# Kernel optimization log

Hardware: AMD Instinct MI355X
Metric: run time of the kernel (lower is better)

Reference implementation:

```python
import jax, jax.numpy as jnp
import numpy as np

N = 100000
E = 300000
IN_C = 256
HID = 256   # 2 * out_channels
OUT_C = 128


def setup_inputs() -> dict:
    key = jax.random.key(0)
    k1, k2, k3, k4, k5 = jax.random.split(key, 5)
    x = jax.random.normal(k1, (N, IN_C), dtype=jnp.float32)
    edge_index = jax.random.randint(k2, (2, E), 0, N, dtype=jnp.int64)
    # Glorot-style init scale for GEMM weights
    W1 = jax.random.normal(k3, (IN_C, HID), dtype=jnp.float32) * (1.0 / np.sqrt(IN_C))
    b1 = jnp.zeros((HID,), dtype=jnp.float32)
    W2 = jax.random.normal(k4, (HID, OUT_C), dtype=jnp.float32) * (1.0 / np.sqrt(HID))
    b2 = jnp.zeros((OUT_C,), dtype=jnp.float32)
    return {"x": x, "edge_index": edge_index, "W1": W1, "b1": b1, "W2": W2, "b2": b2}


def _gcn_conv(x, W, b, src, dst, norm, n_nodes):
    # x: [N, Fin] -> transform then gather-scale-scatter aggregate
    h = x @ W                                   # [N, Fout]
    msgs = h[src] * norm[:, None]               # [E+N, Fout] (includes self-loops)
    out = jax.ops.segment_sum(msgs, dst, num_segments=n_nodes)
    return out + b


def _gcn_norm(edge_index, n_nodes):
    # add self-loops, compute symmetric deg^-1/2 normalization (PyG GCNConv default)
    loops = jnp.arange(n_nodes, dtype=edge_index.dtype)
    src = jnp.concatenate([edge_index[0], loops])
    dst = jnp.concatenate([edge_index[1], loops])
    deg = jax.ops.segment_sum(jnp.ones_like(dst, dtype=jnp.float32), dst, num_segments=n_nodes)
    dinv = jnp.where(deg > 0, jax.lax.rsqrt(deg), 0.0)
    norm = dinv[src] * dinv[dst]                # [E+N]
    return src, dst, norm


def reference(x, edge_index, W1, b1, W2, b2):
    n_nodes = x.shape[0]
    src, dst, norm = _gcn_norm(edge_index, n_nodes)
    h = _gcn_conv(x, W1, b1, src, dst, norm, n_nodes)
    h = jax.nn.relu(h)
    # dropout is identity in eval mode (reference baseline runs deterministic eval)
    return _gcn_conv(h, W2, b2, src, dst, norm, n_nodes)
```

## Files before the change

kernel.cpp:

```cpp
#include <hip/hip_runtime.h>
#include <stdint.h>

#define IN_C  256
#define HID   256
#define OUT_C 128
#define SCAN_BS 1024

typedef __bf16 bf16x8 __attribute__((ext_vector_type(8)));
typedef float  f32x4  __attribute__((ext_vector_type(4)));
typedef unsigned short u16x8 __attribute__((ext_vector_type(8)));
typedef unsigned short u16x4 __attribute__((ext_vector_type(4)));
typedef unsigned short u16x2 __attribute__((ext_vector_type(2)));
typedef unsigned int u32;

static __device__ __forceinline__ unsigned short f2b(float f) {
    union { float f; uint32_t u; } v; v.f = f;
    uint32_t r = v.u + 0x7fffu + ((v.u >> 16) & 1u);
    return (unsigned short)(r >> 16);
}
static __device__ __forceinline__ float b2f(unsigned short b) {
    union { uint32_t u; float f; } v; v.u = ((uint32_t)b) << 16;
    return v.f;
}

typedef __attribute__((address_space(1))) const u32 gas_u32;
typedef __attribute__((address_space(3))) u32 las_u32;
static __device__ __forceinline__ void gld16(const void* g, void* l) {
    __builtin_amdgcn_global_load_lds((gas_u32*)g, (las_u32*)l, 16, 0, 0);
}

__global__ void k_zero_i(int* __restrict__ p, int n) {
    int i = blockIdx.x * blockDim.x + threadIdx.x;
    if (i < n) p[i] = 0;
}

__global__ void k_count(const int* __restrict__ dst, int* __restrict__ cnt, int e) {
    int i = blockIdx.x * blockDim.x + threadIdx.x;
    if (i < e) atomicAdd(&cnt[dst[i]], 1);
}

__global__ __launch_bounds__(SCAN_BS) void k_scan_block(
    const int* __restrict__ cnt, int* __restrict__ rs, int* __restrict__ bsum, int n) {
    __shared__ int s[SCAN_BS];
    const int tid = threadIdx.x;
    const int i = blockIdx.x * SCAN_BS + tid;
    int v = (i < n) ? cnt[i] + 1 : 0;
    s[tid] = v;
    __syncthreads();
    for (int off = 1; off < SCAN_BS; off <<= 1) {
        int t = (tid >= off) ? s[tid - off] : 0;
        __syncthreads();
        s[tid] += t;
        __syncthreads();
    }
    if (i < n) rs[i] = s[tid] - v;
    if (tid == SCAN_BS - 1) bsum[blockIdx.x] = s[tid];
}

__global__ void k_scan_sums(int* __restrict__ bsum, int nb) {
    __shared__ int s[128];
    const int tid = threadIdx.x;
    int v = (tid < nb) ? bsum[tid] : 0;
    s[tid] = v;
    __syncthreads();
    for (int off = 1; off < 128; off <<= 1) {
        int t = (tid >= off) ? s[tid - off] : 0;
        __syncthreads();
        s[tid] += t;
        __syncthreads();
    }
    if (tid < nb) bsum[tid] = s[tid] - v;
}

__global__ void k_scan_add(int* __restrict__ rs, int* __restrict__ cur,
                           const int* __restrict__ bsum, const int* __restrict__ cnt,
                           float* __restrict__ dinv, int2* __restrict__ csrw, int n) {
    int i = blockIdx.x * blockDim.x + threadIdx.x;
    if (i < n) {
        int v = rs[i] + bsum[i >> 10];
        rs[i] = v;
        cur[i] = v + 1;
        float dp1 = (float)(cnt[i] + 1);
        dinv[i] = rsqrtf(dp1);
        csrw[v] = make_int2(i, __float_as_int(1.0f / dp1));
    }
}

__global__ void k_fill(const int* __restrict__ src, const int* __restrict__ dst,
                       const float* __restrict__ dinv,
                       int* __restrict__ cur, int2* __restrict__ csrw, int e) {
    int i = blockIdx.x * blockDim.x + threadIdx.x;
    if (i < e) {
        int s = src[i], d = dst[i];
        int p = atomicAdd(&cur[d], 1);
        csrw[p] = make_int2(s, __float_as_int(dinv[s] * dinv[d]));
    }
}

__global__ void k_prep(const float* __restrict__ W1, const float* __restrict__ W2,
                       unsigned short* __restrict__ W1T, unsigned short* __restrict__ W2T) {
    int i = blockIdx.x * blockDim.x + threadIdx.x;
    if (i < 65536) W1T[i] = f2b(W1[(i & 255) * HID + (i >> 8)]);
    if (i < 32768) W2T[i] = f2b(W2[(i & 255) * OUT_C + (i >> 8)]);
}

__global__ __launch_bounds__(512) void k_gemm1(
    const float* __restrict__ x, const unsigned short* __restrict__ W1T,
    unsigned short* __restrict__ t1, int n) {
    __shared__ __align__(16) unsigned short As[128 * 64];
    __shared__ __align__(16) unsigned short Bs[256 * 64];
    const int tid  = threadIdx.x;
    const int row0 = blockIdx.x * 128;
    const int wid = tid >> 6, lane = tid & 63;
    const int wm = wid >> 2, wn = wid & 3;
    const int lrow = lane & 15, lgrp = lane >> 4;

    f32x4 acc[4][4];
    #pragma unroll
    for (int i = 0; i < 4; ++i)
        #pragma unroll
        for (int j = 0; j < 4; ++j)
            acc[i][j] = (f32x4){0.f, 0.f, 0.f, 0.f};

    for (int kt = 0; kt < 4; ++kt) {
        #pragma unroll
        for (int i = 0; i < 4; ++i) {
            int chunk = tid + 512 * i;
            int nn = chunk >> 3, c = chunk & 7;
            gld16(&W1T[(size_t)nn * 256 + kt * 64 + ((c ^ (nn & 7)) * 8)],
                  &Bs[chunk * 8]);
        }
        #pragma unroll
        for (int i = 0; i < 2; ++i) {
            int chunk = tid + 512 * i;
            int r = chunk >> 3, c = chunk & 7;
            int grow = row0 + r;
            u16x8 pk = {0, 0, 0, 0, 0, 0, 0, 0};
            if (grow < n) {
                const float* sp = x + (size_t)grow * IN_C + kt * 64 + c * 8;
                float4 a = *(const float4*)sp;
                float4 b = *(const float4*)(sp + 4);
                pk[0] = f2b(a.x); pk[1] = f2b(a.y); pk[2] = f2b(a.z); pk[3] = f2b(a.w);
                pk[4] = f2b(b.x); pk[5] = f2b(b.y); pk[6] = f2b(b.z); pk[7] = f2b(b.w);
            }
            *(u16x8*)&As[r * 64 + ((c ^ (r & 7)) * 8)] = pk;
        }
        __syncthreads();
        #pragma unroll
        for (int kk = 0; kk < 2; ++kk) {
            const int cfrag = kk * 4 + lgrp;
            bf16x8 av[4], bv[4];
            #pragma unroll
            for (int mf = 0; mf < 4; ++mf) {
                int r = wm * 64 + mf * 16 + lrow;
                av[mf] = *(const bf16x8*)&As[r * 64 + ((cfrag ^ (r & 7)) * 8)];
            }
            #pragma unroll
            for (int nf = 0; nf < 4; ++nf) {
                int cc = wn * 64 + nf * 16 + lrow;
                bv[nf] = *(const bf16x8*)&Bs[cc * 64 + ((cfrag ^ (cc & 7)) * 8)];
            }
            #pragma unroll
            for (int mf = 0; mf < 4; ++mf)
                #pragma unroll
                for (int nf = 0; nf < 4; ++nf)
                    acc[mf][nf] = __builtin_amdgcn_mfma_f32_16x16x32_bf16(
                        av[mf], bv[nf], acc[mf][nf], 0, 0, 0);
        }
        __syncthreads();
    }
    #pragma unroll
    for (int mf = 0; mf < 4; ++mf)
        #pragma unroll
        for (int j = 0; j < 4; ++j) {
            int grow = row0 + wm * 64 + mf * 16 + lgrp * 4 + j;
            if (grow < n) {
                #pragma unroll
                for (int nf = 0; nf < 4; ++nf) {
                    int col = wn * 64 + nf * 16 + lrow;
                    t1[(size_t)grow * HID + col] = f2b(acc[mf][nf][j]);
                }
            }
        }
}

__global__ __launch_bounds__(256) void k_agg1(
    const unsigned short* __restrict__ t1, const int* __restrict__ rs,
    const int* __restrict__ cnt, const int2* __restrict__ csrw,
    const float* __restrict__ b1, unsigned short* __restrict__ out1, int n) {
    const int w = blockIdx.x * 4 + (threadIdx.x >> 6);
    const int n0 = w * 4;
    if (n0 >= n) return;
    const int lane = threadIdx.x & 63;
    const int ch = lane * 4;
    int beg[4], m[4];
    #pragma unroll
    for (int q = 0; q < 4; ++q) {
        int node = n0 + q;
        bool valid = node < n;
        beg[q] = valid ? rs[node] : 0;
        m[q]   = valid ? cnt[node] + 1 : 0;
    }
    float acc[4][4];
    #pragma unroll
    for (int q = 0; q < 4; ++q)
        #pragma unroll
        for (int k = 0; k < 4; ++k) acc[q][k] = 0.f;
    const int m01 = m[0] > m[1] ? m[0] : m[1];
    const int m23 = m[2] > m[3] ? m[2] : m[3];
    const int mmax = m01 > m23 ? m01 : m23;
    for (int j = 0; j < mmax; ++j) {
        #pragma unroll
        for (int q = 0; q < 4; ++q) {
            if (j < m[q]) {
                int2 p = csrw[beg[q] + j];
                float wq = __int_as_float(p.y);
                u16x4 u = *(const u16x4*)&t1[(size_t)p.x * HID + ch];
                acc[q][0] += b2f(u[0]) * wq; acc[q][1] += b2f(u[1]) * wq;
                acc[q][2] += b2f(u[2]) * wq; acc[q][3] += b2f(u[3]) * wq;
            }
        }
    }
    float4 bb = *(const float4*)(b1 + ch);
    #pragma unroll
    for (int q = 0; q < 4; ++q) {
        int node = n0 + q;
        if (node < n) {
            u16x4 o;
            o[0] = f2b(fmaxf(acc[q][0] + bb.x, 0.f));
            o[1] = f2b(fmaxf(acc[q][1] + bb.y, 0.f));
            o[2] = f2b(fmaxf(acc[q][2] + bb.z, 0.f));
            o[3] = f2b(fmaxf(acc[q][3] + bb.w, 0.f));
            *(u16x4*)&out1[(size_t)node * HID + ch] = o;
        }
    }
}

__global__ __launch_bounds__(256) void k_gemm2(
    const unsigned short* __restrict__ out1, const unsigned short* __restrict__ W2T,
    unsigned short* __restrict__ t2, int n) {
    __shared__ __align__(16) unsigned short As[128 * 64];
    __shared__ __align__(16) unsigned short Bs[128 * 64];
    const int tid  = threadIdx.x;
    const int row0 = blockIdx.x * 128;
    const int wid = tid >> 6, lane = tid & 63;
    const int wm = wid >> 1, wn = wid & 1;
    const int lrow = lane & 15, lgrp = lane >> 4;

    f32x4 acc[4][4];
    #pragma unroll
    for (int i = 0; i < 4; ++i)
        #pragma unroll
        for (int j = 0; j < 4; ++j)
            acc[i][j] = (f32x4){0.f, 0.f, 0.f, 0.f};

    for (int kt = 0; kt < 4; ++kt) {
        #pragma unroll
        for (int i = 0; i < 4; ++i) {
            int chunk = tid + 256 * i;
            int r = chunk >> 3, c = chunk & 7;
            int grow = row0 + r; if (grow > n - 1) grow = n - 1;
            gld16(&out1[(size_t)grow * HID + kt * 64 + ((c ^ (r & 7)) * 8)],
                  &As[chunk * 8]);
        }
        #pragma unroll
        for (int i = 0; i < 4; ++i) {
            int chunk = tid + 256 * i;
            int nn = chunk >> 3, c = chunk & 7;
            gld16(&W2T[(size_t)nn * 256 + kt * 64 + ((c ^ (nn & 7)) * 8)],
                  &Bs[chunk * 8]);
        }
        __syncthreads();
        #pragma unroll
        for (int kk = 0; kk < 2; ++kk) {
            const int cfrag = kk * 4 + lgrp;
            bf16x8 av[4], bv[4];
            #pragma unroll
            for (int mf = 0; mf < 4; ++mf) {
                int r = wm * 64 + mf * 16 + lrow;
                av[mf] = *(const bf16x8*)&As[r * 64 + ((cfrag ^ (r & 7)) * 8)];
            }
            #pragma unroll
            for (int nf = 0; nf < 4; ++nf) {
                int cc = wn * 64 + nf * 16 + lrow;
                bv[nf] = *(const bf16x8*)&Bs[cc * 64 + ((cfrag ^ (cc & 7)) * 8)];
            }
            #pragma unroll
            for (int mf = 0; mf < 4; ++mf)
                #pragma unroll
                for (int nf = 0; nf < 4; ++nf)
                    acc[mf][nf] = __builtin_amdgcn_mfma_f32_16x16x32_bf16(
                        av[mf], bv[nf], acc[mf][nf], 0, 0, 0);
        }
        __syncthreads();
    }
    #pragma unroll
    for (int mf = 0; mf < 4; ++mf)
        #pragma unroll
        for (int j = 0; j < 4; ++j) {
            int grow = row0 + wm * 64 + mf * 16 + lgrp * 4 + j;
            if (grow < n) {
                #pragma unroll
                for (int nf = 0; nf < 4; ++nf) {
                    int col = wn * 64 + nf * 16 + lrow;
                    t2[(size_t)grow * OUT_C + col] = f2b(acc[mf][nf][j]);
                }
            }
        }
}

__global__ __launch_bounds__(256) void k_agg2(
    const unsigned short* __restrict__ t2, const int* __restrict__ rs,
    const int* __restrict__ cnt, const int2* __restrict__ csrw,
    const float* __restrict__ b2, float* __restrict__ out, int n) {
    const int w = blockIdx.x * 4 + (threadIdx.x >> 6);
    const int n0 = w * 4;
    if (n0 >= n) return;
    const int lane = threadIdx.x & 63;
    const int ch = lane * 2;
    int beg[4], m[4];
    #pragma unroll
    for (int q = 0; q < 4; ++q) {
        int node = n0 + q;
        bool valid = node < n;
        beg[q] = valid ? rs[node] : 0;
        m[q]   = valid ? cnt[node] + 1 : 0;
    }
    float acc[4][2];
    #pragma unroll
    for (int q = 0; q < 4; ++q) { acc[q][0] = 0.f; acc[q][1] = 0.f; }
    const int m01 = m[0] > m[1] ? m[0] : m[1];
    const int m23 = m[2] > m[3] ? m[2] : m[3];
    const int mmax = m01 > m23 ? m01 : m23;
    for (int j = 0; j < mmax; ++j) {
        #pragma unroll
        for (int q = 0; q < 4; ++q) {
            if (j < m[q]) {
                int2 p = csrw[beg[q] + j];
                float wq = __int_as_float(p.y);
                u16x2 u = *(const u16x2*)&t2[(size_t)p.x * OUT_C + ch];
                acc[q][0] += b2f(u[0]) * wq; acc[q][1] += b2f(u[1]) * wq;
            }
        }
    }
    float2 bb = *(const float2*)(b2 + ch);
    #pragma unroll
    for (int q = 0; q < 4; ++q) {
        int node = n0 + q;
        if (node < n)
            *(float2*)&out[(size_t)node * OUT_C + ch] =
                make_float2(acc[q][0] + bb.x, acc[q][1] + bb.y);
    }
}

extern "C" void kernel_launch(void* const* d_in, const int* in_sizes, int n_in,
                              void* d_out, int out_size, void* d_ws, size_t ws_size,
                              hipStream_t stream) {
    const float* x  = (const float*)d_in[0];
    const int*   ei = (const int*)d_in[1];
    const float* W1 = (const float*)d_in[2];
    const float* b1 = (const float*)d_in[3];
    const float* W2 = (const float*)d_in[4];
    const float* b2 = (const float*)d_in[5];
    float* out = (float*)d_out;

    const int n = in_sizes[0] / IN_C;
    const int e = in_sizes[1] / 2;
    const int* src = ei;
    const int* dst = ei + e;

    int*   cnt  = (int*)d_ws;
    int*   rs   = cnt + n;
    int*   cur  = rs + n;
    int*   bsum = cur + n;
    float* dinv = (float*)(bsum + 128);
    int2*  csrw = (int2*)(dinv + n);
    unsigned short* W1T = (unsigned short*)(csrw + (size_t)e + n);
    unsigned short* W2T = W1T + 65536;
    unsigned short* t1  = W2T + 32768;
    unsigned short* out1 = t1 + (size_t)n * HID;
    unsigned short* t2  = t1;

    const int nb = (n + SCAN_BS - 1) / SCAN_BS;

    k_zero_i<<<(n + 255) / 256, 256, 0, stream>>>(cnt, n);
    k_count<<<(e + 255) / 256, 256, 0, stream>>>(dst, cnt, e);
    k_scan_block<<<nb, SCAN_BS, 0, stream>>>(cnt, rs, bsum, n);
    k_scan_sums<<<1, 128, 0, stream>>>(bsum, nb);
    k_scan_add<<<(n + 255) / 256, 256, 0, stream>>>(rs, cur, bsum, cnt, dinv, csrw, n);
    k_fill<<<(e + 255) / 256, 256, 0, stream>>>(src, dst, dinv, cur, csrw, e);
    k_prep<<<256, 256, 0, stream>>>(W1, W2, W1T, W2T);

    const int mb = (n + 127) / 128;
    k_gemm1<<<mb, 512, 0, stream>>>(x, W1T, t1, n);
    const int aggblk = (n + 15) / 16;
    k_agg1<<<aggblk, 256, 0, stream>>>(t1, rs, cnt, csrw, b1, out1, n);
    k_gemm2<<<mb, 256, 0, stream>>>(out1, W2T, t2, n);
    k_agg2<<<aggblk, 256, 0, stream>>>(t2, rs, cnt, csrw, b2, out, n);
}
```

Before: 208.8 us.

## Split GEMM1 into 128x128 column tiles, use packed bf16 convert, fuse prep into init

GEMM1 now runs 256-thread blocks that each compute a 128x128 output tile, so there are twice as many blocks and each uses half the LDS for B. Each block still converts its full A tile from fp32, so x is read and converted twice overall. The fp32-to-bf16 conversion of x now uses the v_cvt_pk_bf16_f32 instruction instead of software rounding. Weight transposition moves into the count-zeroing kernel, removing one launch. The trade is more occupancy and parallelism against duplicated x loads and conversion work.

```diff
diff --git a/kernel.cpp b/kernel.cpp
--- a/kernel.cpp
+++ b/kernel.cpp
@@ -22,6 +22,11 @@
     union { uint32_t u; float f; } v; v.u = ((uint32_t)b) << 16;
     return v.f;
 }
+static __device__ __forceinline__ u32 cvtpk(float lo, float hi) {
+    u32 r;
+    asm("v_cvt_pk_bf16_f32 %0, %1, %2" : "=v"(r) : "v"(lo), "v"(hi));
+    return r;
+}
 
 typedef __attribute__((address_space(1))) const u32 gas_u32;
 typedef __attribute__((address_space(3))) u32 las_u32;
@@ -29,9 +34,13 @@
     __builtin_amdgcn_global_load_lds((gas_u32*)g, (las_u32*)l, 16, 0, 0);
 }
 
-__global__ void k_zero_i(int* __restrict__ p, int n) {
+__global__ void k_init(const float* __restrict__ W1, const float* __restrict__ W2,
+                       unsigned short* __restrict__ W1T, unsigned short* __restrict__ W2T,
+                       int* __restrict__ cnt, int n) {
     int i = blockIdx.x * blockDim.x + threadIdx.x;
-    if (i < n) p[i] = 0;
+    if (i < 65536) W1T[i] = f2b(W1[(i & 255) * HID + (i >> 8)]);
+    if (i < 32768) W2T[i] = f2b(W2[(i & 255) * OUT_C + (i >> 8)]);
+    if (i < n) cnt[i] = 0;
 }
 
 __global__ void k_count(const int* __restrict__ dst, int* __restrict__ cnt, int e) {
@@ -97,22 +106,16 @@
     }
 }
 
-__global__ void k_prep(const float* __restrict__ W1, const float* __restrict__ W2,
-                       unsigned short* __restrict__ W1T, unsigned short* __restrict__ W2T) {
-    int i = blockIdx.x * blockDim.x + threadIdx.x;
-    if (i < 65536) W1T[i] = f2b(W1[(i & 255) * HID + (i >> 8)]);
-    if (i < 32768) W2T[i] = f2b(W2[(i & 255) * OUT_C + (i >> 8)]);
-}
-
-__global__ __launch_bounds__(512) void k_gemm1(
+__global__ __launch_bounds__(256) void k_gemm1(
     const float* __restrict__ x, const unsigned short* __restrict__ W1T,
     unsigned short* __restrict__ t1, int n) {
     __shared__ __align__(16) unsigned short As[128 * 64];
-    __shared__ __align__(16) unsigned short Bs[256 * 64];
+    __shared__ __align__(16) unsigned short Bs[128 * 64];
     const int tid  = threadIdx.x;
-    const int row0 = blockIdx.x * 128;
+    const int bm = blockIdx.x >> 1, bn = blockIdx.x & 1;
+    const int row0 = bm * 128, col0 = bn * 128;
     const int wid = tid >> 6, lane = tid & 63;
-    const int wm = wid >> 2, wn = wid & 3;
+    const int wm = wid >> 1, wn = wid & 1;
     const int lrow = lane & 15, lgrp = lane >> 4;
 
     f32x4 acc[4][4];
@@ -125,25 +128,26 @@
     for (int kt = 0; kt < 4; ++kt) {
         #pragma unroll
         for (int i = 0; i < 4; ++i) {
-            int chunk = tid + 512 * i;
+            int chunk = tid + 256 * i;
             int nn = chunk >> 3, c = chunk & 7;
-            gld16(&W1T[(size_t)nn * 256 + kt * 64 + ((c ^ (nn & 7)) * 8)],
+            gld16(&W1T[(size_t)(col0 + nn) * 256 + kt * 64 + ((c ^ (nn & 7)) * 8)],
                   &Bs[chunk * 8]);
         }
         #pragma unroll
-        for (int i = 0; i < 2; ++i) {
-            int chunk = tid + 512 * i;
+        for (int i = 0; i < 4; ++i) {
+            int chunk = tid + 256 * i;
             int r = chunk >> 3, c = chunk & 7;
             int grow = row0 + r;
-            u16x8 pk = {0, 0, 0, 0, 0, 0, 0, 0};
+            union { u32 w[4]; u16x8 v; } pk;
+            pk.w[0] = 0; pk.w[1] = 0; pk.w[2] = 0; pk.w[3] = 0;
             if (grow < n) {
                 const float* sp = x + (size_t)grow * IN_C + kt * 64 + c * 8;
-                float4 a = *(const float4*)sp;
-                float4 b = *(const float4*)(sp + 4);
-                pk[0] = f2b(a.x); pk[1] = f2b(a.y); pk[2] = f2b(a.z); pk[3] = f2b(a.w);
-                pk[4] = f2b(b.x); pk[5] = f2b(b.y); pk[6] = f2b(b.z); pk[7] = f2b(b.w);
-            }
-            *(u16x8*)&As[r * 64 + ((c ^ (r & 7)) * 8)] = pk;
+                f32x4 a = *(const f32x4*)sp;
+                f32x4 b = *(const f32x4*)(sp + 4);
+                pk.w[0] = cvtpk(a[0], a[1]); pk.w[1] = cvtpk(a[2], a[3]);
+                pk.w[2] = cvtpk(b[0], b[1]); pk.w[3] = cvtpk(b[2], b[3]);
+            }
+            *(u16x8*)&As[r * 64 + ((c ^ (r & 7)) * 8)] = pk.v;
         }
         __syncthreads();
         #pragma unroll
@@ -177,7 +181,7 @@
             if (grow < n) {
                 #pragma unroll
                 for (int nf = 0; nf < 4; ++nf) {
-                    int col = wn * 64 + nf * 16 + lrow;
+                    int col = col0 + wn * 64 + nf * 16 + lrow;
                     t1[(size_t)grow * HID + col] = f2b(acc[mf][nf][j]);
                 }
             }
@@ -383,16 +387,15 @@
 
     const int nb = (n + SCAN_BS - 1) / SCAN_BS;
 
-    k_zero_i<<<(n + 255) / 256, 256, 0, stream>>>(cnt, n);
+    k_init<<<(n + 255) / 256, 256, 0, stream>>>(W1, W2, W1T, W2T, cnt, n);
     k_count<<<(e + 255) / 256, 256, 0, stream>>>(dst, cnt, e);
     k_scan_block<<<nb, SCAN_BS, 0, stream>>>(cnt, rs, bsum, n);
     k_scan_sums<<<1, 128, 0, stream>>>(bsum, nb);
     k_scan_add<<<(n + 255) / 256, 256, 0, stream>>>(rs, cur, bsum, cnt, dinv, csrw, n);
     k_fill<<<(e + 255) / 256, 256, 0, stream>>>(src, dst, dinv, cur, csrw, e);
-    k_prep<<<256, 256, 0, stream>>>(W1, W2, W1T, W2T);
 
     const int mb = (n + 127) / 128;
-    k_gemm1<<<mb, 512, 0, stream>>>(x, W1T, t1, n);
+    k_gemm1<<<mb * 2, 256, 0, stream>>>(x, W1T, t1, n);
     const int aggblk = (n + 15) / 16;
     k_agg1<<<aggblk, 256, 0, stream>>>(t1, rs, cnt, csrw, b1, out1, n);
     k_gemm2<<<mb, 256, 0, stream>>>(out1, W2T, t2, n);
```

After: 218.1 us. 1.04x slower.
